# Performance work log

Measured on AMD Instinct MI355X. Metric: run time of the kernel, lower is better.

Reference implementation:

```python
import jax, jax.numpy as jnp
import numpy as np

B, S, E, H = 4, 2048, 1024, 16
D = E // H  # head dim = 64


def setup_inputs() -> dict:
    key = jax.random.key(0)
    ks = jax.random.split(key, 5)
    scale = 1.0 / np.sqrt(E)
    return {
        "x": jax.random.normal(ks[0], (B, S, E), dtype=jnp.float32),
        "Wq": jax.random.normal(ks[1], (E, E), dtype=jnp.float32) * scale,
        "Wk": jax.random.normal(ks[2], (E, E), dtype=jnp.float32) * scale,
        "Wv": jax.random.normal(ks[3], (E, E), dtype=jnp.float32) * scale,
        "Wo": jax.random.normal(ks[4], (E, E), dtype=jnp.float32) * scale,
    }


def reference(x, Wq, Wk, Wv, Wo):
    # Projections (no bias), then split heads: tf.split(axis=-1)+concat(axis=0)
    # is equivalent to reshape (B,S,H,D) -> (B,H,S,D) per-head attention.
    def heads(t):
        return t.reshape(B, S, H, D).transpose(0, 2, 1, 3)  # [B,H,S,D]

    q = heads(x @ Wq)
    k = heads(x @ Wk)
    v = heads(x @ Wv)

    inv_sqrt_d = 1.0 / jnp.sqrt(jnp.float32(E / H))
    scores = jnp.einsum("bhqd,bhkd->bhqk", q, k) * inv_sqrt_d  # [B,H,S,S]
    attn = jax.nn.softmax(scores, axis=-1)
    ctx = jnp.einsum("bhqk,bhkd->bhqd", attn, v)  # [B,H,S,D]
    ctx = ctx.transpose(0, 2, 1, 3).reshape(B, S, E)  # merge heads
    return ctx @ Wo
```

## Files before the change

### kernel.cpp

```cpp
#include <hip/hip_runtime.h>

#define BB 4
#define SS 2048
#define EE 1024
#define HH 16
#define DD 64
#define MM (BB*SS)

typedef __bf16 bf16_t;
typedef bf16_t bf16x8 __attribute__((ext_vector_type(8)));
typedef bf16_t bf16x4 __attribute__((ext_vector_type(4)));
typedef float  f32x4  __attribute__((ext_vector_type(4)));
typedef float  f32x16 __attribute__((ext_vector_type(16)));
typedef unsigned int u32;

#define GLDS16(g, l) __builtin_amdgcn_global_load_lds( \
    (const __attribute__((address_space(1))) void*)(g), \
    (__attribute__((address_space(3))) void*)(l), 16, 0, 0)

static __device__ inline u32 pk2(float a, float b) {
    union { bf16_t h; unsigned short u; } x, y;
    x.h = (bf16_t)a; y.h = (bf16_t)b;
    return ((u32)y.u << 16) | x.u;
}


__global__ __launch_bounds__(256) void cast_x_kernel(const float* __restrict__ in,
                                                     bf16_t* __restrict__ out, int n4) {
    int i = blockIdx.x * 256 + threadIdx.x;
    if (i >= n4) return;
    float4 v = ((const float4*)in)[i];
    bf16x4 o;
    o[0] = (bf16_t)v.x; o[1] = (bf16_t)v.y; o[2] = (bf16_t)v.z; o[3] = (bf16_t)v.w;
    ((bf16x4*)out)[i] = o;
}

__global__ __launch_bounds__(256) void cast_wT_kernel(const float* __restrict__ W,
                                                      bf16_t* __restrict__ Wt) {
    __shared__ float tile[32][33];
    int bx = blockIdx.x, by = blockIdx.y;
    int tx = threadIdx.x, ty = threadIdx.y;
    #pragma unroll
    for (int i = 0; i < 32; i += 8)
        tile[ty + i][tx] = W[(size_t)(by*32 + ty + i)*EE + bx*32 + tx];
    __syncthreads();
    #pragma unroll
    for (int i = 0; i < 32; i += 8)
        Wt[(size_t)(bx*32 + ty + i)*EE + by*32 + tx] = (bf16_t)tile[tx][ty + i];
}

template<int EPI, int GX, int GY>
__global__ __launch_bounds__(256) void gemm_bt(const bf16_t* __restrict__ A,
                                               const bf16_t* __restrict__ Bt,
                                               void* __restrict__ Cout) {
    constexpr int K = 1024;
    constexpr int NWG = GX * GY, QW = NWG / 8;
    __shared__ __align__(16) bf16_t Al[128 * 64];
    __shared__ __align__(16) bf16_t Bl[128 * 64];

    int hw = blockIdx.y * GX + blockIdx.x;
    int L  = (hw & 7) * QW + (hw >> 3);
    int R0 = (L / GX) * 128, C0 = (L % GX) * 128;

    int t = threadIdx.x, lane = t & 63, wid = t >> 6;
    int wr = wid >> 1, wc = wid & 1, lr = lane & 15, lg = lane >> 4;

    const int sr8 = lane >> 3;
    const int ssw = ((lane & 7) ^ sr8) * 8;
    const bf16_t* Ag = A  + (size_t)(R0 + wid*32 + sr8) * K + ssw;
    const bf16_t* Bg = Bt + (size_t)(C0 + wid*32 + sr8) * K + ssw;

    f32x4 acc[4][4];
    #pragma unroll
    for (int m = 0; m < 4; ++m)
        #pragma unroll
        for (int n = 0; n < 4; ++n)
            acc[m][n] = (f32x4){0.f, 0.f, 0.f, 0.f};

    for (int k0 = 0; k0 < K; k0 += 64) {
        __syncthreads();
        #pragma unroll
        for (int i = 0; i < 4; ++i) {
            GLDS16(Ag + (size_t)(i*8) * K + k0, &Al[(wid*32 + i*8) * 64]);
            GLDS16(Bg + (size_t)(i*8) * K + k0, &Bl[(wid*32 + i*8) * 64]);
        }
        __syncthreads();
        #pragma unroll
        for (int kk = 0; kk < 2; ++kk) {
            bf16x8 af[4], bfr[4];
            #pragma unroll
            for (int m = 0; m < 4; ++m) {
                int rr = wr*64 + m*16 + lr;
                af[m] = *(bf16x8*)&Al[rr*64 + (((kk*4 + lg) ^ (lr & 7)) * 8)];
            }
            #pragma unroll
            for (int n = 0; n < 4; ++n) {
                int rr = wc*64 + n*16 + lr;
                bfr[n] = *(bf16x8*)&Bl[rr*64 + (((kk*4 + lg) ^ (lr & 7)) * 8)];
            }
            #pragma unroll
            for (int m = 0; m < 4; ++m)
                #pragma unroll
                for (int n = 0; n < 4; ++n)
                    acc[m][n] = __builtin_amdgcn_mfma_f32_16x16x32_bf16(af[m], bfr[n], acc[m][n], 0, 0, 0);
        }
    }

    #pragma unroll
    for (int m = 0; m < 4; ++m) {
        int row0 = R0 + wr*64 + m*16 + lg*4;
        #pragma unroll
        for (int n = 0; n < 4; ++n) {
            int col = C0 + wc*64 + n*16 + lr;
            #pragma unroll
            for (int r = 0; r < 4; ++r) {
                int row = row0 + r;
                float v = acc[m][n][r];
                if constexpr (EPI == 4) {
                    int sel = col >> 10, cc = col & 1023;
                    float vv = sel ? v : v * 0.125f;
                    int b = row >> 11, s = row & 2047, hh = cc >> 6, d = cc & 63;
                    ((bf16_t*)Cout)[(size_t)sel * MM * EE +
                                    ((size_t)(b*HH + hh)*SS + s)*DD + d] = (bf16_t)vv;
                } else if constexpr (EPI == 1) {
                    ((float*)Cout)[(size_t)row * EE + col] = v;
                } else {
                    int hh = row >> 6, d = row & 63, b = col >> 11, s = col & 2047;
                    ((bf16_t*)Cout)[(((size_t)(b*HH + hh)*DD + d))*SS + s] = (bf16_t)v;
                }
            }
        }
    }
}

__global__ __launch_bounds__(256) void attn_kernel(const bf16_t* __restrict__ Q,
                                                   const bf16_t* __restrict__ K,
                                                   const bf16_t* __restrict__ Vt,
                                                   bf16_t* __restrict__ Cb) {
    __shared__ __align__(16) bf16_t Kl[2][64 * 64];
    __shared__ __align__(16) bf16_t Vl[2][64 * 64];
    __shared__ float fsb[4][32];

    const int t = threadIdx.x, lane = t & 63, w = t >> 6;
    const int c = lane & 31, h = lane >> 5;

    const int hwb = blockIdx.y * 16 + blockIdx.x;
    const int Lb  = (hwb & 7) * 128 + (hwb >> 3);
    const int bh  = Lb >> 4;
    const int qx  = Lb & 15;
    const int qg = qx * 128 + w * 32 + c;

    const bf16_t* Qh = Q  + (size_t)bh * SS * DD;
    const bf16_t* Kh = K  + (size_t)bh * SS * DD;
    const bf16_t* Vh = Vt + (size_t)bh * DD * SS;

    bf16x8 qf[4];
    #pragma unroll
    for (int ds = 0; ds < 4; ++ds)
        qf[ds] = *(const bf16x8*)&Qh[(size_t)qg * DD + ds*16 + h*8];

    f32x16 O0, O1;
    #pragma unroll
    for (int i = 0; i < 16; ++i) { O0[i] = 0.f; O1[i] = 0.f; }
    float lsum = 0.f;

    const int srow = lane >> 3;
    const int ssw  = ((lane & 7) ^ srow) << 3;
    const bf16_t* Kst = Kh + (size_t)(w*16 + srow) * DD + ssw;
    const bf16_t* Vst = Vh + (size_t)(w*16 + srow) * SS + ssw;

    #define STAGE(bufi, t0) do { \
        GLDS16(Kst + (size_t)(t0) * DD, &Kl[bufi][(w*16)*64]); \
        GLDS16(Kst + (size_t)((t0) + 8) * DD, &Kl[bufi][(w*16 + 8)*64]); \
        GLDS16(Vst + (t0), &Vl[bufi][(w*16)*64]); \
        GLDS16(Vst + 8*SS + (t0), &Vl[bufi][(w*16 + 8)*64]); \
    } while (0)

    STAGE(0, 0);
    __syncthreads();

    int buf = 0;
    for (int tt = 0; tt < SS/64; ++tt) {
        if (tt + 1 < SS/64) STAGE(buf ^ 1, (tt + 1) * 64);

        const bf16_t* KB = Kl[buf];
        const bf16_t* VB = Vl[buf];

        f32x16 s0, s1;
        #pragma unroll
        for (int i = 0; i < 16; ++i) { s0[i] = 0.f; s1[i] = 0.f; }
        __builtin_amdgcn_s_setprio(1);
        #pragma unroll
        for (int ds = 0; ds < 4; ++ds) {
            int qd = ((ds*2 + h) ^ (c & 7)) << 3;
            bf16x8 k0 = *(const bf16x8*)&KB[(c << 6) + qd];
            bf16x8 k1 = *(const bf16x8*)&KB[((32 + c) << 6) + qd];
            s0 = __builtin_amdgcn_mfma_f32_32x32x16_bf16(k0, qf[ds], s0, 0, 0, 0);
            s1 = __builtin_amdgcn_mfma_f32_32x32x16_bf16(k1, qf[ds], s1, 0, 0, 0);
        }
        __builtin_amdgcn_s_setprio(0);

        float rs = 0.f;
        #pragma unroll
        for (int i = 0; i < 16; ++i) { s0[i] = __expf(s0[i]); rs += s0[i]; }
        #pragma unroll
        for (int i = 0; i < 16; ++i) { s1[i] = __expf(s1[i]); rs += s1[i]; }
        rs += __shfl_xor(rs, 32);
        lsum += rs;

        u32 wk0[4][2], wk1[4][2];
        #pragma unroll
        for (int g = 0; g < 4; ++g) {
            wk0[g][0] = pk2(s0[g*4 + 0], s0[g*4 + 1]);
            wk0[g][1] = pk2(s0[g*4 + 2], s0[g*4 + 3]);
            wk1[g][0] = pk2(s1[g*4 + 0], s1[g*4 + 1]);
            wk1[g][1] = pk2(s1[g*4 + 2], s1[g*4 + 3]);
        }

        __builtin_amdgcn_s_setprio(1);
        #pragma unroll
        for (int kb = 0; kb < 2; ++kb) {
            #pragma unroll
            for (int ks = 0; ks < 2; ++ks) {
                u32 a0 = kb ? wk1[2*ks][0]     : wk0[2*ks][0];
                u32 a1 = kb ? wk1[2*ks][1]     : wk0[2*ks][1];
                u32 b0 = kb ? wk1[2*ks + 1][0] : wk0[2*ks + 1][0];
                u32 b1 = kb ? wk1[2*ks + 1][1] : wk0[2*ks + 1][1];
                u32 keep0 = h ? b0 : a0, keep1 = h ? b1 : a1;
                u32 send0 = h ? a0 : b0, send1 = h ? a1 : b1;
                u32 r0 = (u32)__shfl_xor((int)send0, 32);
                u32 r1 = (u32)__shfl_xor((int)send1, 32);
                union { u32 d[4]; bf16x8 v; } af;
                if (h == 0) { af.d[0] = keep0; af.d[1] = keep1; af.d[2] = r0; af.d[3] = r1; }
                else        { af.d[0] = r0;    af.d[1] = r1;    af.d[2] = keep0; af.d[3] = keep1; }

                int qd = ((kb*4 + ks*2 + h) ^ (c & 7)) << 3;
                bf16x8 v0 = *(const bf16x8*)&VB[(c << 6) + qd];
                bf16x8 v1 = *(const bf16x8*)&VB[((32 + c) << 6) + qd];
                O0 = __builtin_amdgcn_mfma_f32_32x32x16_bf16(af.v, v0, O0, 0, 0, 0);
                O1 = __builtin_amdgcn_mfma_f32_32x32x16_bf16(af.v, v1, O1, 0, 0, 0);
            }
        }
        __builtin_amdgcn_s_setprio(0);

        __syncthreads();
        buf ^= 1;
    }

    if (lane < 32) fsb[w][c] = lsum;
    int b = bh >> 4, hh = bh & 15;
    #pragma unroll
    for (int r = 0; r < 16; ++r) {
        int rowp = (r & 3) + ((r >> 2) << 3) + (h << 2);
        int qrow = qx * 128 + w * 32 + rowp;
        float inv = 1.f / fsb[w][rowp];
        size_t base = ((size_t)(b*SS + qrow)) * EE + hh * DD;
        Cb[base + c]      = (bf16_t)(O0[r] * inv);
        Cb[base + 32 + c] = (bf16_t)(O1[r] * inv);
    }
    #undef STAGE
}


extern "C" void kernel_launch(void* const* d_in, const int* in_sizes, int n_in,
                              void* d_out, int out_size, void* d_ws, size_t ws_size,
                              hipStream_t stream) {
    const float* x  = (const float*)d_in[0];
    const float* Wq = (const float*)d_in[1];
    const float* Wk = (const float*)d_in[2];
    const float* Wv = (const float*)d_in[3];
    const float* Wo = (const float*)d_in[4];

    bf16_t* xb  = (bf16_t*)d_ws;
    bf16_t* WqT = xb  + (size_t)MM * EE;
    bf16_t* WkT = WqT + (size_t)EE * EE;
    bf16_t* WvT = WkT + (size_t)EE * EE;
    bf16_t* WoT = WvT + (size_t)EE * EE;
    bf16_t* Qb  = WoT + (size_t)EE * EE;
    bf16_t* Kb  = Qb  + (size_t)MM * EE;
    bf16_t* Vtg = Kb  + (size_t)MM * EE;
    bf16_t* Cb  = Vtg + (size_t)MM * EE;

    cast_x_kernel<<<dim3(MM * EE / 4 / 256), dim3(256), 0, stream>>>(x, xb, MM * EE / 4);
    dim3 tg(32, 32), tb(32, 8);
    cast_wT_kernel<<<tg, tb, 0, stream>>>(Wq, WqT);
    cast_wT_kernel<<<tg, tb, 0, stream>>>(Wk, WkT);
    cast_wT_kernel<<<tg, tb, 0, stream>>>(Wv, WvT);
    cast_wT_kernel<<<tg, tb, 0, stream>>>(Wo, WoT);

    gemm_bt<4, 16, 64><<<dim3(16, 64), dim3(256), 0, stream>>>(xb, WqT, (void*)Qb);
    gemm_bt<2, 64, 8><<<dim3(64, 8), dim3(256), 0, stream>>>(WvT, xb, (void*)Vtg);

    attn_kernel<<<dim3(SS / 128, BB * HH), dim3(256), 0, stream>>>(Qb, Kb, Vtg, Cb);

    gemm_bt<1, 8, 64><<<dim3(8, 64), dim3(256), 0, stream>>>(Cb, WoT, d_out);
}
```

Measured before the change: 305.4 us.

## Double-buffer GEMM LDS tiles, use raw exp2 with folded log2e, permlane swaps

The projection GEMM now double-buffers its LDS tiles, so the global-to-LDS loads for the next K slice are issued before the MFMAs on the current slice and one barrier per iteration is dropped. In attention, the Q scaling constant now includes log2(e), which lets the softmax call the hardware v_exp_f32 (base 2) directly instead of __expf. The cross-half P exchange now uses v_permlane32_swap instead of two shuffles plus selects. The cost is doubled GEMM LDS use, which may lower occupancy, and inline asm that bypasses compiler scheduling.

```diff
diff --git a/kernel.cpp b/kernel.cpp
--- a/kernel.cpp
+++ b/kernel.cpp
@@ -17,6 +17,10 @@
 #define GLDS16(g, l) __builtin_amdgcn_global_load_lds( \
     (const __attribute__((address_space(1))) void*)(g), \
     (__attribute__((address_space(3))) void*)(l), 16, 0, 0)
+
+static __device__ inline float ex2(float x) {
+    float r; asm("v_exp_f32 %0, %1" : "=v"(r) : "v"(x)); return r;
+}
 
 static __device__ inline u32 pk2(float a, float b) {
     union { bf16_t h; unsigned short u; } x, y;
@@ -55,8 +59,8 @@
                                                void* __restrict__ Cout) {
     constexpr int K = 1024;
     constexpr int NWG = GX * GY, QW = NWG / 8;
-    __shared__ __align__(16) bf16_t Al[128 * 64];
-    __shared__ __align__(16) bf16_t Bl[128 * 64];
+    __shared__ __align__(16) bf16_t Al[2][128 * 64];
+    __shared__ __align__(16) bf16_t Bl[2][128 * 64];
 
     int hw = blockIdx.y * GX + blockIdx.x;
     int L  = (hw & 7) * QW + (hw >> 3);
@@ -77,26 +81,34 @@
         for (int n = 0; n < 4; ++n)
             acc[m][n] = (f32x4){0.f, 0.f, 0.f, 0.f};
 
+    #pragma unroll
+    for (int i = 0; i < 4; ++i) {
+        GLDS16(Ag + (size_t)(i*8) * K, &Al[0][(wid*32 + i*8) * 64]);
+        GLDS16(Bg + (size_t)(i*8) * K, &Bl[0][(wid*32 + i*8) * 64]);
+    }
+    __syncthreads();
+
+    int bi = 0;
     for (int k0 = 0; k0 < K; k0 += 64) {
-        __syncthreads();
-        #pragma unroll
-        for (int i = 0; i < 4; ++i) {
-            GLDS16(Ag + (size_t)(i*8) * K + k0, &Al[(wid*32 + i*8) * 64]);
-            GLDS16(Bg + (size_t)(i*8) * K + k0, &Bl[(wid*32 + i*8) * 64]);
-        }
-        __syncthreads();
+        if (k0 + 64 < K) {
+            #pragma unroll
+            for (int i = 0; i < 4; ++i) {
+                GLDS16(Ag + (size_t)(i*8) * K + k0 + 64, &Al[bi^1][(wid*32 + i*8) * 64]);
+                GLDS16(Bg + (size_t)(i*8) * K + k0 + 64, &Bl[bi^1][(wid*32 + i*8) * 64]);
+            }
+        }
         #pragma unroll
         for (int kk = 0; kk < 2; ++kk) {
             bf16x8 af[4], bfr[4];
             #pragma unroll
             for (int m = 0; m < 4; ++m) {
                 int rr = wr*64 + m*16 + lr;
-                af[m] = *(bf16x8*)&Al[rr*64 + (((kk*4 + lg) ^ (lr & 7)) * 8)];
+                af[m] = *(bf16x8*)&Al[bi][rr*64 + (((kk*4 + lg) ^ (lr & 7)) * 8)];
             }
             #pragma unroll
             for (int n = 0; n < 4; ++n) {
                 int rr = wc*64 + n*16 + lr;
-                bfr[n] = *(bf16x8*)&Bl[rr*64 + (((kk*4 + lg) ^ (lr & 7)) * 8)];
+                bfr[n] = *(bf16x8*)&Bl[bi][rr*64 + (((kk*4 + lg) ^ (lr & 7)) * 8)];
             }
             #pragma unroll
             for (int m = 0; m < 4; ++m)
@@ -104,6 +116,8 @@
                 for (int n = 0; n < 4; ++n)
                     acc[m][n] = __builtin_amdgcn_mfma_f32_16x16x32_bf16(af[m], bfr[n], acc[m][n], 0, 0, 0);
         }
+        __syncthreads();
+        bi ^= 1;
     }
 
     #pragma unroll
@@ -118,7 +132,7 @@
                 float v = acc[m][n][r];
                 if constexpr (EPI == 4) {
                     int sel = col >> 10, cc = col & 1023;
-                    float vv = sel ? v : v * 0.125f;
+                    float vv = sel ? v : v * 0.18033688011112042f;
                     int b = row >> 11, s = row & 2047, hh = cc >> 6, d = cc & 63;
                     ((bf16_t*)Cout)[(size_t)sel * MM * EE +
                                     ((size_t)(b*HH + hh)*SS + s)*DD + d] = (bf16_t)vv;
@@ -202,9 +216,9 @@
 
         float rs = 0.f;
         #pragma unroll
-        for (int i = 0; i < 16; ++i) { s0[i] = __expf(s0[i]); rs += s0[i]; }
-        #pragma unroll
-        for (int i = 0; i < 16; ++i) { s1[i] = __expf(s1[i]); rs += s1[i]; }
+        for (int i = 0; i < 16; ++i) { s0[i] = ex2(s0[i]); rs += s0[i]; }
+        #pragma unroll
+        for (int i = 0; i < 16; ++i) { s1[i] = ex2(s1[i]); rs += s1[i]; }
         rs += __shfl_xor(rs, 32);
         lsum += rs;
 
@@ -222,17 +236,14 @@
         for (int kb = 0; kb < 2; ++kb) {
             #pragma unroll
             for (int ks = 0; ks < 2; ++ks) {
-                u32 a0 = kb ? wk1[2*ks][0]     : wk0[2*ks][0];
-                u32 a1 = kb ? wk1[2*ks][1]     : wk0[2*ks][1];
-                u32 b0 = kb ? wk1[2*ks + 1][0] : wk0[2*ks + 1][0];
-                u32 b1 = kb ? wk1[2*ks + 1][1] : wk0[2*ks + 1][1];
-                u32 keep0 = h ? b0 : a0, keep1 = h ? b1 : a1;
-                u32 send0 = h ? a0 : b0, send1 = h ? a1 : b1;
-                u32 r0 = (u32)__shfl_xor((int)send0, 32);
-                u32 r1 = (u32)__shfl_xor((int)send1, 32);
+                u32 x0 = kb ? wk1[2*ks][0]     : wk0[2*ks][0];
+                u32 x1 = kb ? wk1[2*ks + 1][0] : wk0[2*ks + 1][0];
+                u32 y0 = kb ? wk1[2*ks][1]     : wk0[2*ks][1];
+                u32 y1 = kb ? wk1[2*ks + 1][1] : wk0[2*ks + 1][1];
+                asm("v_permlane32_swap_b32 %0, %1" : "+v"(x0), "+v"(x1));
+                asm("v_permlane32_swap_b32 %0, %1" : "+v"(y0), "+v"(y1));
                 union { u32 d[4]; bf16x8 v; } af;
-                if (h == 0) { af.d[0] = keep0; af.d[1] = keep1; af.d[2] = r0; af.d[3] = r1; }
-                else        { af.d[0] = r0;    af.d[1] = r1;    af.d[2] = keep0; af.d[3] = keep1; }
+                af.d[0] = x0; af.d[1] = y0; af.d[2] = x1; af.d[3] = y1;
 
                 int qd = ((kb*4 + ks*2 + h) ^ (c & 7)) << 3;
                 bf16x8 v0 = *(const bf16x8*)&VB[(c << 6) + qd];
```

Result: faster. 289.7 us (-5.1%).
